# Kernel tuning notes

Measured on AMD Instinct MI355X. Metric: run time of the kernel, lower is better.

Reference implementation:

```python
import jax, jax.numpy as jnp
from jax import lax
import numpy as np

N_FEAT = 131072
N_TARGET = 2048
N_LATENT = 64
INNER_STEPS = 2
EPS = 1e-7


def setup_inputs() -> dict:
    key = jax.random.key(0)
    ks = jax.random.split(key, 10)
    x = jax.random.normal(ks[0], (N_FEAT,), jnp.float32)
    y = jax.random.normal(ks[1], (N_TARGET,), jnp.float32)
    mu_x = jax.random.normal(ks[2], (N_FEAT,), jnp.float32) * 0.01
    mu_y = jax.random.normal(ks[3], (N_TARGET,), jnp.float32) * 0.01
    u0 = jax.random.normal(ks[4], (N_LATENT,), jnp.float32)
    u = u0 / jnp.sqrt(jnp.sum(u0 * u0))
    Wz = jax.random.normal(ks[5], (N_LATENT, N_FEAT), jnp.float32) * 0.1
    Cz = jax.random.normal(ks[6], (N_LATENT, N_TARGET), jnp.float32) * 0.1
    t_sq_sum = jax.random.uniform(ks[7], (N_LATENT,), jnp.float32) * 10.0 + 1.0
    bz = jax.random.normal(ks[8], (N_LATENT,), jnp.float32) * 0.1
    P = jax.random.normal(ks[9], (N_LATENT, N_FEAT), jnp.float32) * 0.1
    return {"x": x, "y": y, "mu_x": mu_x, "mu_y": mu_y, "u": u, "Wz": Wz,
            "Cz": Cz, "t_sq_sum": t_sq_sum, "bz": bz, "P": P, "n": 100}


def _one_pass(u_i, wz_row, cz_row, tss, xc, yc):
    # one NIPALS inner iteration for latent i
    wz = wz_row + xc * u_i
    tz = jnp.dot(xc, wz) / (jnp.sqrt(jnp.sum(wz * wz)) + EPS)
    tss_ = tss + tz * tz
    t = tz / jnp.sqrt(tss_)
    cz = cz_row + yc * t
    C_i = cz / jnp.sqrt(jnp.sum(cz * cz))
    u_new = jnp.dot(yc, C_i)
    return u_new, wz, tz, tss_, t, cz, C_i


def reference(x, y, mu_x, mu_y, u, Wz, Cz, t_sq_sum, bz, P, n):
    # functional translation of IPLS.partial_fit (post burn-in branch, n > burn_in)
    nf = jnp.float32(n)
    mu_x_new = mu_x * (nf / (nf + 1.0)) + x / (nf + 1.0)
    mu_y_new = mu_y * (nf / (nf + 1.0)) + y / (nf + 1.0)
    xc = x - mu_x_new  # centered sample [n_feat]
    yc = y - mu_y_new  # centered target [n_target]

    def latent_step(carry, row):
        xc, yc = carry
        u_i, wz_row, cz_row, tss, bz_i, p_row = row
        u_i, wz, tz, tss_, t, cz, C_i = _one_pass(u_i, wz_row, cz_row, tss, xc, yc)
        for _ in range(INNER_STEPS - 1):
            u_i, wz, tz, tss_, t, cz, C_i = _one_pass(u_i, wz_row, cz_row, tss, xc, yc)
        bz_new = bz_i + u_i * tz
        b = bz_new / jnp.sqrt(tss_)
        p_new = p_row + xc * t
        xc = xc - t * p_new          # deflate x
        yc = yc - b * t * C_i        # deflate y
        return (xc, yc), (u_i, wz, cz, tss_, bz_new, p_new)

    (_, _), outs = lax.scan(latent_step, (xc, yc), (u, Wz, Cz, t_sq_sum, bz, P))
    u_new, Wz_new, Cz_new, tss_new, bz_new, P_new = outs
    return (mu_x_new, mu_y_new, u_new, Wz_new, Cz_new, tss_new, bz_new, P_new)
```

## Files before the change

kernel.cpp:

```cpp
#include <hip/hip_runtime.h>


#define NF 131072
#define NT 2048
#define NL 64

#define PSIZE 8385
#define NBX 512
#define NBY 16
#define NMID 32
#define REDK 16
#define BK 128
#define LDST 68
#define NBEX 256
#define NBEY 4

#define O_MUX 0
#define O_MUY 131072
#define O_U   133120
#define O_WZ  133184
#define O_CZ  8521792
#define O_TSS 8652864
#define O_BZ  8652928
#define O_P   8652992

#define W_FINX 0
#define W_FINY 8385
#define W_COEF 16770

__global__ __launch_bounds__(256) void gram_partial(
    const float* __restrict__ PX, const float* __restrict__ WzX,
    const float* __restrict__ xsX, const float* __restrict__ musX,
    const float* __restrict__ CzY, const float* __restrict__ ysY,
    const float* __restrict__ musY, const int* __restrict__ np,
    float* __restrict__ partX, float* __restrict__ voutX,
    float* __restrict__ partY, float* __restrict__ voutY)
{
    __shared__ float lds[2 * BK * LDST + BK];
    float* ldsA = lds;
    float* ldsB = lds + BK * LDST;
    float* ldsV = lds + 2 * BK * LDST;

    const bool isX = (int)blockIdx.x < NBX;
    const float* A   = isX ? PX   : CzY;
    const float* B   = isX ? WzX  : CzY;
    const float* xs  = isX ? xsX  : ysY;
    const float* mus = isX ? musX : musY;
    float* part      = isX ? partX : partY;
    float* vout      = isX ? voutX : voutY;
    const int K   = isX ? NF : NT;
    const int KC  = isX ? (NF / NBX) : (NT / NBY);
    const int bid = isX ? (int)blockIdx.x : (int)blockIdx.x - NBX;

    const int t    = threadIdx.x;
    const int w    = t >> 6;
    const int lane = t & 63;
    const int j0   = lane & 56;
    const int i0   = (lane & 7) << 3;

    const float nf = (float)(*np);
    const float r  = nf / (nf + 1.f);

    float accPW[8][8], accPP[8][8];
    float accXW[8], accXP[8], accW2[8], accS0 = 0.f;
#pragma unroll
    for (int s = 0; s < 8; ++s) {
        accXW[s] = 0.f; accXP[s] = 0.f; accW2[s] = 0.f;
#pragma unroll
        for (int q = 0; q < 8; ++q) { accPW[s][q] = 0.f; accPP[s][q] = 0.f; }
    }

    const int kbase  = bid * KC;
    const int ntiles = KC / BK;
    const int c4     = ((t >> 3) & 31) << 2;
    const int rlow   = t & 7;

    for (int tile = 0; tile < ntiles; ++tile) {
        const int k0 = kbase + tile * BK;
        if (tile) __syncthreads();
#pragma unroll
        for (int m = 0; m < 8; ++m) {
            int row = rlow | (m << 3);
            const float4 av = *(const float4*)(A + (size_t)row * K + (k0 + c4));
            const float4 bv = *(const float4*)(B + (size_t)row * K + (k0 + c4));
            ldsA[(c4 + 0) * LDST + row] = av.x;
            ldsA[(c4 + 1) * LDST + row] = av.y;
            ldsA[(c4 + 2) * LDST + row] = av.z;
            ldsA[(c4 + 3) * LDST + row] = av.w;
            ldsB[(c4 + 0) * LDST + row] = bv.x;
            ldsB[(c4 + 1) * LDST + row] = bv.y;
            ldsB[(c4 + 2) * LDST + row] = bv.z;
            ldsB[(c4 + 3) * LDST + row] = bv.w;
        }
        if (t < BK) {
            float val = r * (xs[k0 + t] - mus[k0 + t]);
            ldsV[t] = val;
            vout[k0 + t] = val;
        }
        __syncthreads();

        const int kend = w * 32 + 32;
        for (int kk = w * 32; kk < kend; ++kk) {
            const float* bA = ldsA + kk * LDST;
            const float* bB = ldsB + kk * LDST;
            float4 a0 = *(const float4*)(bA + j0);
            float4 a1 = *(const float4*)(bA + j0 + 4);
            float4 b0 = *(const float4*)(bB + i0);
            float4 b1 = *(const float4*)(bB + i0 + 4);
            float4 c0 = *(const float4*)(bA + i0);
            float4 c1 = *(const float4*)(bA + i0 + 4);
            float aj[8] = {a0.x,a0.y,a0.z,a0.w,a1.x,a1.y,a1.z,a1.w};
            float bi[8] = {b0.x,b0.y,b0.z,b0.w,b1.x,b1.y,b1.z,b1.w};
            float ci[8] = {c0.x,c0.y,c0.z,c0.w,c1.x,c1.y,c1.z,c1.w};
#pragma unroll
            for (int s = 0; s < 8; ++s)
#pragma unroll
                for (int q = 0; q < 8; ++q) {
                    accPW[s][q] = fmaf(aj[s], bi[q], accPW[s][q]);
                    accPP[s][q] = fmaf(aj[s], ci[q], accPP[s][q]);
                }
            float vv = ldsV[kk];
            if (j0 == 0) {
#pragma unroll
                for (int q = 0; q < 8; ++q) accXW[q] = fmaf(vv, bi[q], accXW[q]);
            }
            if (j0 == 8) {
#pragma unroll
                for (int q = 0; q < 8; ++q) accW2[q] = fmaf(bi[q], bi[q], accW2[q]);
            }
            if (i0 == 0) {
#pragma unroll
                for (int s = 0; s < 8; ++s) accXP[s] = fmaf(vv, aj[s], accXP[s]);
            }
            if (lane == 16) accS0 = fmaf(vv, vv, accS0);
        }
    }
    __syncthreads();

    float* red = lds;
    float* po  = part + (size_t)bid * PSIZE;
#pragma unroll
    for (int s = 0; s < 8; ++s)
#pragma unroll
        for (int q = 0; q < 8; ++q)
            red[w * 4096 + (j0 + s) * 64 + (i0 + q)] = accPW[s][q];
    __syncthreads();
    for (int o = t; o < 4096; o += 256)
        po[o] = red[o] + red[4096 + o] + red[8192 + o] + red[12288 + o];
    __syncthreads();
#pragma unroll
    for (int s = 0; s < 8; ++s)
#pragma unroll
        for (int q = 0; q < 8; ++q)
            red[w * 4096 + (j0 + s) * 64 + (i0 + q)] = accPP[s][q];
    __syncthreads();
    for (int o = t; o < 4096; o += 256)
        po[4096 + o] = red[o] + red[4096 + o] + red[8192 + o] + red[12288 + o];
    __syncthreads();
    if (j0 == 0) {
#pragma unroll
        for (int q = 0; q < 8; ++q) red[w * 193 + (i0 + q)] = accXW[q];
    }
    if (i0 == 0) {
#pragma unroll
        for (int s = 0; s < 8; ++s) red[w * 193 + 64 + (j0 + s)] = accXP[s];
    }
    if (j0 == 8) {
#pragma unroll
        for (int q = 0; q < 8; ++q) red[w * 193 + 128 + (i0 + q)] = accW2[q];
    }
    if (lane == 16) red[w * 193 + 192] = accS0;
    __syncthreads();
    for (int o = t; o < 193; o += 256)
        po[8192 + o] = red[o] + red[193 + o] + red[386 + o] + red[579 + o];
}

__global__ __launch_bounds__(256) void gram_reduceA(
    const float* __restrict__ partX, float* __restrict__ mid)
{
    int ob = (int)blockIdx.x % 33;
    int kb = (int)blockIdx.x / 33;
    int o  = ob * 256 + threadIdx.x;
    if (o >= PSIZE) return;
    const float* p = partX + (size_t)kb * REDK * PSIZE + o;
    float s = 0.f;
#pragma unroll
    for (int k = 0; k < REDK; ++k) s += p[(size_t)k * PSIZE];
    mid[(size_t)kb * PSIZE + o] = s;
}

__global__ __launch_bounds__(256) void gram_reduceB(
    const float* __restrict__ mid, const float* __restrict__ partY,
    float* __restrict__ finX, float* __restrict__ finY)
{
    int b = blockIdx.x;
    float s = 0.f;
    float* fin; int o;
    if (b < 33) {
        o = b * 256 + threadIdx.x;
        if (o >= PSIZE) return;
        fin = finX;
#pragma unroll
        for (int k = 0; k < NMID; ++k) s += mid[(size_t)k * PSIZE + o];
    } else {
        o = (b - 33) * 256 + threadIdx.x;
        if (o >= PSIZE) return;
        fin = finY;
#pragma unroll
        for (int k = 0; k < NBY; ++k) s += partY[(size_t)k * PSIZE + o];
    }
    if (o < 4096) {
        int j = o >> 6, i = o & 63;
        fin[(i << 6) + j] = s;
    } else if (o < 8192) {
        int q = o - 4096;
        int j = q >> 6, i = q & 63;
        fin[4096 + (i << 6) + j] = s;
    } else {
        fin[o] = s;
    }
}

__global__ __launch_bounds__(256) void recursion(
    const float* __restrict__ finX, const float* __restrict__ finY,
    const float* __restrict__ u_in, const float* __restrict__ tss_in,
    const float* __restrict__ bz_in,
    float* __restrict__ out_u, float* __restrict__ out_tss, float* __restrict__ out_bz,
    float* __restrict__ coef)
{
    __shared__ float lx[PSIZE];
    __shared__ float ly[PSIZE];
    __shared__ float lsc[3 * NL];

    const int t = threadIdx.x;
    for (int o = t; o < PSIZE; o += 256) { lx[o] = finX[o]; ly[o] = finY[o]; }
    if (t < NL) {
        lsc[t]          = u_in[t];
        lsc[NL + t]     = tss_in[t];
        lsc[2 * NL + t] = bz_in[t];
    }
    __syncthreads();
    if (t >= 64) return;
    const int lane = t;

    const float* PWt = lx;
    const float* PPt = lx + 4096;
    const float* XW  = lx + 8192;
    const float* XP  = lx + 8256;
    const float* W2  = lx + 8320;
    const float* CCt = ly;
    const float* YC  = ly + 8192;

    float beta = 0.f, delta = 0.f;
    float alpha = 1.f, gamma = 1.f;
    float s  = lx[8384];
    float sy = ly[8384];

    float rPW = PWt[lane], rPP = PPt[lane], rCC = CCt[lane];

    for (int i = 0; i < NL; ++i) {
        int inext = (i + 1) & 63;
        float nPW = PWt[inext * 64 + lane];
        float nPP = PPt[inext * 64 + lane];
        float nCC = CCt[inext * 64 + lane];

        float v0 = beta * rPW, v1 = beta * rPP, v2 = delta * rCC;
#pragma unroll
        for (int off = 32; off; off >>= 1) {
            v0 += __shfl_xor(v0, off);
            v1 += __shfl_xor(v1, off);
            v2 += __shfl_xor(v2, off);
        }
        float a  = alpha * XW[i] + v0;
        float d  = alpha * XP[i] + v1;
        float ay = gamma * YC[i] + v2;
        float ppii = __shfl(rPP, i);
        float c2   = __shfl(rCC, i);
        float w2   = W2[i];
        float u0 = lsc[i], tss0 = lsc[NL + i], bzi = lsc[2 * NL + i];

        float den1 = sqrtf(fmaxf(w2 + 2.f * u0 * a + u0 * u0 * s, 0.f)) + 1e-7f;
        float tz1  = (a + u0 * s) / den1;
        float tss1 = tss0 + tz1 * tz1;
        float t1   = tz1 / sqrtf(tss1);
        float cn1  = sqrtf(fmaxf(c2 + 2.f * t1 * ay + t1 * t1 * sy, 0.f));
        float u1   = (ay + t1 * sy) / cn1;
        float den2  = sqrtf(fmaxf(w2 + 2.f * u1 * a + u1 * u1 * s, 0.f)) + 1e-7f;
        float tz2   = (a + u1 * s) / den2;
        float tss2  = tss0 + tz2 * tz2;
        float st2   = sqrtf(tss2);
        float t2    = tz2 / st2;
        float cn2sq = fmaxf(c2 + 2.f * t2 * ay + t2 * t2 * sy, 0.f);
        float cn2   = sqrtf(cn2sq);
        float u2    = (ay + t2 * sy) / cn2;
        float bzo   = bzi + u2 * tz2;
        float b     = bzo / st2;
        float g     = b * t2 / cn2;

        if (lane == 0) {
            out_u[i]   = u2;
            out_tss[i] = tss2;
            out_bz[i]  = bzo;
            coef[i]            = u1;
            coef[NL + i]       = t2;
            coef[2 * NL + i]   = g;
        }

        float f  = 1.f - t2 * t2;
        float fy = 1.f - g * t2;
        s  = f * f * s - 2.f * f * t2 * d + t2 * t2 * ppii;
        sy = sy - 2.f * g * (ay + t2 * sy) + g * g * cn2sq;
        beta  *= f;  if (lane == i) beta  = -t2;
        delta *= fy; if (lane == i) delta = -g;
        alpha *= f;
        gamma *= fy;

        rPW = nPW; rPP = nPP; rCC = nCC;
    }
}

__global__ __launch_bounds__(128) void expand(
    const float* __restrict__ P, const float* __restrict__ Wz,
    const float* __restrict__ x, const float* __restrict__ Cz,
    const float* __restrict__ y, const float* __restrict__ coef,
    float* __restrict__ xc0_mux,
    float* __restrict__ yc0_muy,
    float* __restrict__ outW, float* __restrict__ outP, float* __restrict__ outC)
{
    __shared__ float cA[NL], cB[NL];
    const int t = threadIdx.x;
    const int b = (int)blockIdx.x;

    if (b < NBEX) {
        if (t < NL) { cA[t] = coef[t]; cB[t] = coef[NL + t]; }
        const int c = (b * 128 + t) << 2;
        float4 xc = *(const float4*)(xc0_mux + c);
        float4 xv = *(const float4*)(x + c);
        float4 mu;
        mu.x = xv.x - xc.x; mu.y = xv.y - xc.y;
        mu.z = xv.z - xc.z; mu.w = xv.w - xc.w;
        *(float4*)(xc0_mux + c) = mu;
        __syncthreads();
#pragma unroll 8
        for (int i = 0; i < NL; ++i) {
            size_t off = (size_t)i * NF + c;
            float4 wv = *(const float4*)(Wz + off);
            float4 pv = *(const float4*)(P + off);
            float u1 = cA[i], t2 = cB[i];
            wv.x = fmaf(u1, xc.x, wv.x); wv.y = fmaf(u1, xc.y, wv.y);
            wv.z = fmaf(u1, xc.z, wv.z); wv.w = fmaf(u1, xc.w, wv.w);
            pv.x = fmaf(t2, xc.x, pv.x); pv.y = fmaf(t2, xc.y, pv.y);
            pv.z = fmaf(t2, xc.z, pv.z); pv.w = fmaf(t2, xc.w, pv.w);
            *(float4*)(outW + off) = wv;
            *(float4*)(outP + off) = pv;
            xc.x = fmaf(-t2, pv.x, xc.x); xc.y = fmaf(-t2, pv.y, xc.y);
            xc.z = fmaf(-t2, pv.z, xc.z); xc.w = fmaf(-t2, pv.w, xc.w);
        }
    } else {
        if (t < NL) { cA[t] = coef[NL + t]; cB[t] = coef[2 * NL + t]; }
        const int c = ((b - NBEX) * 128 + t) << 2;
        float4 yc = *(const float4*)(yc0_muy + c);
        float4 yv = *(const float4*)(y + c);
        float4 mu;
        mu.x = yv.x - yc.x; mu.y = yv.y - yc.y;
        mu.z = yv.z - yc.z; mu.w = yv.w - yc.w;
        *(float4*)(yc0_muy + c) = mu;
        __syncthreads();
#pragma unroll 8
        for (int i = 0; i < NL; ++i) {
            size_t off = (size_t)i * NT + c;
            float4 cv = *(const float4*)(Cz + off);
            float t2 = cA[i], g = cB[i];
            cv.x = fmaf(t2, yc.x, cv.x); cv.y = fmaf(t2, yc.y, cv.y);
            cv.z = fmaf(t2, yc.z, cv.z); cv.w = fmaf(t2, yc.w, cv.w);
            *(float4*)(outC + off) = cv;
            yc.x = fmaf(-g, cv.x, yc.x); yc.y = fmaf(-g, cv.y, yc.y);
            yc.z = fmaf(-g, cv.z, yc.z); yc.w = fmaf(-g, cv.w, yc.w);
        }
    }
}

extern "C" void kernel_launch(void* const* d_in, const int* in_sizes, int n_in,
                              void* d_out, int out_size, void* d_ws, size_t ws_size,
                              hipStream_t stream)
{
    (void)in_sizes; (void)n_in; (void)out_size; (void)ws_size;

    const float* x    = (const float*)d_in[0];
    const float* y    = (const float*)d_in[1];
    const float* mu_x = (const float*)d_in[2];
    const float* mu_y = (const float*)d_in[3];
    const float* u    = (const float*)d_in[4];
    const float* Wz   = (const float*)d_in[5];
    const float* Cz   = (const float*)d_in[6];
    const float* tss  = (const float*)d_in[7];
    const float* bz   = (const float*)d_in[8];
    const float* P    = (const float*)d_in[9];
    const int*   n    = (const int*)d_in[10];

    float* out = (float*)d_out;
    float* ws  = (float*)d_ws;

    float* xc0   = out + O_MUX;
    float* yc0   = out + O_MUY;
    float* partX = out + O_P;
    float* partY = partX + (size_t)NBX * PSIZE;
    float* mid   = partY + (size_t)NBY * PSIZE;
    float* finX  = ws + W_FINX;
    float* finY  = ws + W_FINY;
    float* coef  = ws + W_COEF;

    gram_partial<<<NBX + NBY, 256, 0, stream>>>(P, Wz, x, mu_x,
                                                Cz, y, mu_y, n,
                                                partX, xc0, partY, yc0);

    gram_reduceA<<<33 * NMID, 256, 0, stream>>>(partX, mid);
    gram_reduceB<<<66, 256, 0, stream>>>(mid, partY, finX, finY);

    recursion<<<1, 256, 0, stream>>>(finX, finY, u, tss, bz,
                                     out + O_U, out + O_TSS, out + O_BZ, coef);

    expand<<<NBEX + NBEY, 128, 0, stream>>>(P, Wz, x, Cz, y, coef,
                                            xc0, yc0,
                                            out + O_WZ, out + O_P, out + O_CZ);
}
```

Measured before the change: 261.1 us.

## Double gram partial blocks, rework recursion with readlane, and scalarize expand

The X gram pass now runs on 1024 blocks with a 64-wide k tile and occupancy hints, and the Y gram moves to a separate launch. The partial buffers are split across two output regions, and reduceB drops its transpose by writing results in natural order. The recursion replaces shuffle reductions with incrementally updated per-lane vectors, uses readlane broadcasts and fast rcp/rsq approximations, and writes outputs once at the end. The expand kernel switches from float4 to scalar accesses with 256 threads per block. Together these aim for more parallelism and a shorter serial recursion, at the cost of more partial traffic and slight precision loss from the approximate reciprocals.

```diff
diff --git a/kernel.cpp b/kernel.cpp
--- a/kernel.cpp
+++ b/kernel.cpp
@@ -6,14 +6,12 @@
 #define NL 64
 
 #define PSIZE 8385
-#define NBX 512
+#define NBX 1024
 #define NBY 16
-#define NMID 32
+#define NMID 64
 #define REDK 16
-#define BK 128
+#define BK 64
 #define LDST 68
-#define NBEX 256
-#define NBEY 4
 
 #define O_MUX 0
 #define O_MUY 131072
@@ -28,29 +26,23 @@
 #define W_FINY 8385
 #define W_COEF 16770
 
-__global__ __launch_bounds__(256) void gram_partial(
-    const float* __restrict__ PX, const float* __restrict__ WzX,
-    const float* __restrict__ xsX, const float* __restrict__ musX,
-    const float* __restrict__ CzY, const float* __restrict__ ysY,
-    const float* __restrict__ musY, const int* __restrict__ np,
-    float* __restrict__ partX, float* __restrict__ voutX,
-    float* __restrict__ partY, float* __restrict__ voutY)
+__device__ __forceinline__ float rdlane(float v, int l) {
+    return __int_as_float(__builtin_amdgcn_readlane(__float_as_int(v), l));
+}
+#define FRCP(x) __builtin_amdgcn_rcpf(x)
+#define FRSQ(x) __builtin_amdgcn_rsqf(x)
+
+__global__ __launch_bounds__(256, 4) void gram_partial(
+    const float* __restrict__ A, const float* __restrict__ B,
+    const float* __restrict__ xs, const float* __restrict__ mus,
+    const int* __restrict__ np, int K, int KC,
+    float* __restrict__ part0, float* __restrict__ part1,
+    float* __restrict__ vout)
 {
     __shared__ float lds[2 * BK * LDST + BK];
     float* ldsA = lds;
     float* ldsB = lds + BK * LDST;
     float* ldsV = lds + 2 * BK * LDST;
-
-    const bool isX = (int)blockIdx.x < NBX;
-    const float* A   = isX ? PX   : CzY;
-    const float* B   = isX ? WzX  : CzY;
-    const float* xs  = isX ? xsX  : ysY;
-    const float* mus = isX ? musX : musY;
-    float* part      = isX ? partX : partY;
-    float* vout      = isX ? voutX : voutY;
-    const int K   = isX ? NF : NT;
-    const int KC  = isX ? (NF / NBX) : (NT / NBY);
-    const int bid = isX ? (int)blockIdx.x : (int)blockIdx.x - NBX;
 
     const int t    = threadIdx.x;
     const int w    = t >> 6;
@@ -70,17 +62,18 @@
         for (int q = 0; q < 8; ++q) { accPW[s][q] = 0.f; accPP[s][q] = 0.f; }
     }
 
+    const int bid    = (int)blockIdx.x;
     const int kbase  = bid * KC;
     const int ntiles = KC / BK;
-    const int c4     = ((t >> 3) & 31) << 2;
-    const int rlow   = t & 7;
+    const int rbase = (t & 7) | ((t >> 4) & 8);
+    const int c4    = ((t >> 3) & 15) << 2;
 
     for (int tile = 0; tile < ntiles; ++tile) {
         const int k0 = kbase + tile * BK;
         if (tile) __syncthreads();
 #pragma unroll
-        for (int m = 0; m < 8; ++m) {
-            int row = rlow | (m << 3);
+        for (int m = 0; m < 4; ++m) {
+            int row = rbase | (m << 4);
             const float4 av = *(const float4*)(A + (size_t)row * K + (k0 + c4));
             const float4 bv = *(const float4*)(B + (size_t)row * K + (k0 + c4));
             ldsA[(c4 + 0) * LDST + row] = av.x;
@@ -99,8 +92,8 @@
         }
         __syncthreads();
 
-        const int kend = w * 32 + 32;
-        for (int kk = w * 32; kk < kend; ++kk) {
+        const int kend = w * 16 + 16;
+        for (int kk = w * 16; kk < kend; ++kk) {
             const float* bA = ldsA + kk * LDST;
             const float* bB = ldsB + kk * LDST;
             float4 a0 = *(const float4*)(bA + j0);
@@ -138,24 +131,51 @@
     __syncthreads();
 
     float* red = lds;
-    float* po  = part + (size_t)bid * PSIZE;
-#pragma unroll
-    for (int s = 0; s < 8; ++s)
-#pragma unroll
-        for (int q = 0; q < 8; ++q)
-            red[w * 4096 + (j0 + s) * 64 + (i0 + q)] = accPW[s][q];
-    __syncthreads();
-    for (int o = t; o < 4096; o += 256)
-        po[o] = red[o] + red[4096 + o] + red[8192 + o] + red[12288 + o];
-    __syncthreads();
-#pragma unroll
-    for (int s = 0; s < 8; ++s)
-#pragma unroll
-        for (int q = 0; q < 8; ++q)
-            red[w * 4096 + (j0 + s) * 64 + (i0 + q)] = accPP[s][q];
-    __syncthreads();
-    for (int o = t; o < 4096; o += 256)
-        po[4096 + o] = red[o] + red[4096 + o] + red[8192 + o] + red[12288 + o];
+    float* po  = (bid < 512 ? part0 : part1) + (size_t)(bid & 511) * PSIZE;
+
+    if (j0 < 32) {
+#pragma unroll
+        for (int s = 0; s < 8; ++s)
+#pragma unroll
+            for (int q = 0; q < 8; ++q)
+                red[w * 2048 + (j0 + s) * 64 + (i0 + q)] = accPW[s][q];
+    }
+    __syncthreads();
+    for (int o = t; o < 2048; o += 256)
+        po[o] = red[o] + red[2048 + o] + red[4096 + o] + red[6144 + o];
+    __syncthreads();
+    if (j0 >= 32) {
+#pragma unroll
+        for (int s = 0; s < 8; ++s)
+#pragma unroll
+            for (int q = 0; q < 8; ++q)
+                red[w * 2048 + (j0 - 32 + s) * 64 + (i0 + q)] = accPW[s][q];
+    }
+    __syncthreads();
+    for (int o = t; o < 2048; o += 256)
+        po[2048 + o] = red[o] + red[2048 + o] + red[4096 + o] + red[6144 + o];
+    __syncthreads();
+    if (j0 < 32) {
+#pragma unroll
+        for (int s = 0; s < 8; ++s)
+#pragma unroll
+            for (int q = 0; q < 8; ++q)
+                red[w * 2048 + (j0 + s) * 64 + (i0 + q)] = accPP[s][q];
+    }
+    __syncthreads();
+    for (int o = t; o < 2048; o += 256)
+        po[4096 + o] = red[o] + red[2048 + o] + red[4096 + o] + red[6144 + o];
+    __syncthreads();
+    if (j0 >= 32) {
+#pragma unroll
+        for (int s = 0; s < 8; ++s)
+#pragma unroll
+            for (int q = 0; q < 8; ++q)
+                red[w * 2048 + (j0 - 32 + s) * 64 + (i0 + q)] = accPP[s][q];
+    }
+    __syncthreads();
+    for (int o = t; o < 2048; o += 256)
+        po[6144 + o] = red[o] + red[2048 + o] + red[4096 + o] + red[6144 + o];
     __syncthreads();
     if (j0 == 0) {
 #pragma unroll
@@ -176,13 +196,15 @@
 }
 
 __global__ __launch_bounds__(256) void gram_reduceA(
-    const float* __restrict__ partX, float* __restrict__ mid)
+    const float* __restrict__ part0, const float* __restrict__ part1,
+    float* __restrict__ mid)
 {
     int ob = (int)blockIdx.x % 33;
     int kb = (int)blockIdx.x / 33;
     int o  = ob * 256 + threadIdx.x;
     if (o >= PSIZE) return;
-    const float* p = partX + (size_t)kb * REDK * PSIZE + o;
+    const float* p = (kb < 32 ? part0 : part1)
+                   + (size_t)((kb & 31) * REDK) * PSIZE + o;
     float s = 0.f;
 #pragma unroll
     for (int k = 0; k < REDK; ++k) s += p[(size_t)k * PSIZE];
@@ -194,30 +216,20 @@
     float* __restrict__ finX, float* __restrict__ finY)
 {
     int b = blockIdx.x;
-    float s = 0.f;
-    float* fin; int o;
     if (b < 33) {
-        o = b * 256 + threadIdx.x;
+        int o = b * 256 + threadIdx.x;
         if (o >= PSIZE) return;
-        fin = finX;
+        float s = 0.f;
 #pragma unroll
         for (int k = 0; k < NMID; ++k) s += mid[(size_t)k * PSIZE + o];
+        finX[o] = s;
     } else {
-        o = (b - 33) * 256 + threadIdx.x;
+        int o = (b - 33) * 256 + threadIdx.x;
         if (o >= PSIZE) return;
-        fin = finY;
+        float s = 0.f;
 #pragma unroll
         for (int k = 0; k < NBY; ++k) s += partY[(size_t)k * PSIZE + o];
-    }
-    if (o < 4096) {
-        int j = o >> 6, i = o & 63;
-        fin[(i << 6) + j] = s;
-    } else if (o < 8192) {
-        int q = o - 4096;
-        int j = q >> 6, i = q & 63;
-        fin[4096 + (i << 6) + j] = s;
-    } else {
-        fin[o] = s;
+        finY[o] = s;
     }
 }
 
@@ -243,83 +255,81 @@
     if (t >= 64) return;
     const int lane = t;
 
-    const float* PWt = lx;
-    const float* PPt = lx + 4096;
-    const float* XW  = lx + 8192;
-    const float* XP  = lx + 8256;
-    const float* W2  = lx + 8320;
-    const float* CCt = ly;
-    const float* YC  = ly + 8192;
-
-    float beta = 0.f, delta = 0.f;
-    float alpha = 1.f, gamma = 1.f;
+    const float* PW = lx;
+    const float* PP = lx + 4096;
+    const float* CC = ly;
+
+    float A   = lx[8192 + lane];
+    float D   = lx[8256 + lane];
+    float AY  = ly[8192 + lane];
+    float w2r = lx[8320 + lane];
+    float u0r = lsc[lane], tssr = lsc[NL + lane], bzr = lsc[2 * NL + lane];
     float s  = lx[8384];
     float sy = ly[8384];
 
-    float rPW = PWt[lane], rPP = PPt[lane], rCC = CCt[lane];
+    float rPW = PW[lane], rPP = PP[lane], rCC = CC[lane];
+    float o_u = 0.f, o_tss = 0.f, o_bz = 0.f, o_u1 = 0.f, o_t2 = 0.f, o_g = 0.f;
 
     for (int i = 0; i < NL; ++i) {
         int inext = (i + 1) & 63;
-        float nPW = PWt[inext * 64 + lane];
-        float nPP = PPt[inext * 64 + lane];
-        float nCC = CCt[inext * 64 + lane];
-
-        float v0 = beta * rPW, v1 = beta * rPP, v2 = delta * rCC;
-#pragma unroll
-        for (int off = 32; off; off >>= 1) {
-            v0 += __shfl_xor(v0, off);
-            v1 += __shfl_xor(v1, off);
-            v2 += __shfl_xor(v2, off);
-        }
-        float a  = alpha * XW[i] + v0;
-        float d  = alpha * XP[i] + v1;
-        float ay = gamma * YC[i] + v2;
-        float ppii = __shfl(rPP, i);
-        float c2   = __shfl(rCC, i);
-        float w2   = W2[i];
-        float u0 = lsc[i], tss0 = lsc[NL + i], bzi = lsc[2 * NL + i];
+        float nPW = PW[inext * 64 + lane];
+        float nPP = PP[inext * 64 + lane];
+        float nCC = CC[inext * 64 + lane];
+
+        float a    = rdlane(A, i);
+        float d    = rdlane(D, i);
+        float ay   = rdlane(AY, i);
+        float ppii = rdlane(rPP, i);
+        float c2   = rdlane(rCC, i);
+        float w2   = rdlane(w2r, i);
+        float u0   = rdlane(u0r, i);
+        float tss0 = rdlane(tssr, i);
+        float bzi  = rdlane(bzr, i);
 
         float den1 = sqrtf(fmaxf(w2 + 2.f * u0 * a + u0 * u0 * s, 0.f)) + 1e-7f;
-        float tz1  = (a + u0 * s) / den1;
+        float tz1  = (a + u0 * s) * FRCP(den1);
         float tss1 = tss0 + tz1 * tz1;
-        float t1   = tz1 / sqrtf(tss1);
+        float t1   = tz1 * FRSQ(tss1);
         float cn1  = sqrtf(fmaxf(c2 + 2.f * t1 * ay + t1 * t1 * sy, 0.f));
-        float u1   = (ay + t1 * sy) / cn1;
+        float u1   = (ay + t1 * sy) * FRCP(cn1);
         float den2  = sqrtf(fmaxf(w2 + 2.f * u1 * a + u1 * u1 * s, 0.f)) + 1e-7f;
-        float tz2   = (a + u1 * s) / den2;
+        float tz2   = (a + u1 * s) * FRCP(den2);
         float tss2  = tss0 + tz2 * tz2;
-        float st2   = sqrtf(tss2);
-        float t2    = tz2 / st2;
+        float rs2   = FRSQ(tss2);
+        float t2    = tz2 * rs2;
         float cn2sq = fmaxf(c2 + 2.f * t2 * ay + t2 * t2 * sy, 0.f);
         float cn2   = sqrtf(cn2sq);
-        float u2    = (ay + t2 * sy) / cn2;
+        float rcn2  = FRCP(cn2);
+        float u2    = (ay + t2 * sy) * rcn2;
         float bzo   = bzi + u2 * tz2;
-        float b     = bzo / st2;
-        float g     = b * t2 / cn2;
-
-        if (lane == 0) {
-            out_u[i]   = u2;
-            out_tss[i] = tss2;
-            out_bz[i]  = bzo;
-            coef[i]            = u1;
-            coef[NL + i]       = t2;
-            coef[2 * NL + i]   = g;
+        float b     = bzo * rs2;
+        float g     = b * t2 * rcn2;
+
+        if (lane == i) {
+            o_u = u2; o_tss = tss2; o_bz = bzo;
+            o_u1 = u1; o_t2 = t2; o_g = g;
         }
 
         float f  = 1.f - t2 * t2;
         float fy = 1.f - g * t2;
         s  = f * f * s - 2.f * f * t2 * d + t2 * t2 * ppii;
         sy = sy - 2.f * g * (ay + t2 * sy) + g * g * cn2sq;
-        beta  *= f;  if (lane == i) beta  = -t2;
-        delta *= fy; if (lane == i) delta = -g;
-        alpha *= f;
-        gamma *= fy;
+        A  = fmaf(-t2, rPW, f * A);
+        D  = fmaf(-t2, rPP, f * D);
+        AY = fmaf(-g,  rCC, fy * AY);
 
         rPW = nPW; rPP = nPP; rCC = nCC;
     }
-}
-
-__global__ __launch_bounds__(128) void expand(
+
+    out_u[lane]   = o_u;
+    out_tss[lane] = o_tss;
+    out_bz[lane]  = o_bz;
+    coef[lane]          = o_u1;
+    coef[NL + lane]     = o_t2;
+    coef[2 * NL + lane] = o_g;
+}
+
+__global__ __launch_bounds__(256) void expand(
     const float* __restrict__ P, const float* __restrict__ Wz,
     const float* __restrict__ x, const float* __restrict__ Cz,
     const float* __restrict__ y, const float* __restrict__ coef,
@@ -331,51 +341,35 @@
     const int t = threadIdx.x;
     const int b = (int)blockIdx.x;
 
-    if (b < NBEX) {
+    if (b < 512) {
         if (t < NL) { cA[t] = coef[t]; cB[t] = coef[NL + t]; }
-        const int c = (b * 128 + t) << 2;
-        float4 xc = *(const float4*)(xc0_mux + c);
-        float4 xv = *(const float4*)(x + c);
-        float4 mu;
-        mu.x = xv.x - xc.x; mu.y = xv.y - xc.y;
-        mu.z = xv.z - xc.z; mu.w = xv.w - xc.w;
-        *(float4*)(xc0_mux + c) = mu;
+        const int c = b * 256 + t;
+        float xc = xc0_mux[c];
+        xc0_mux[c] = x[c] - xc;
         __syncthreads();
 #pragma unroll 8
         for (int i = 0; i < NL; ++i) {
             size_t off = (size_t)i * NF + c;
-            float4 wv = *(const float4*)(Wz + off);
-            float4 pv = *(const float4*)(P + off);
-            float u1 = cA[i], t2 = cB[i];
-            wv.x = fmaf(u1, xc.x, wv.x); wv.y = fmaf(u1, xc.y, wv.y);
-            wv.z = fmaf(u1, xc.z, wv.z); wv.w = fmaf(u1, xc.w, wv.w);
-            pv.x = fmaf(t2, xc.x, pv.x); pv.y = fmaf(t2, xc.y, pv.y);
-            pv.z = fmaf(t2, xc.z, pv.z); pv.w = fmaf(t2, xc.w, pv.w);
-            *(float4*)(outW + off) = wv;
-            *(float4*)(outP + off) = pv;
-            xc.x = fmaf(-t2, pv.x, xc.x); xc.y = fmaf(-t2, pv.y, xc.y);
-            xc.z = fmaf(-t2, pv.z, xc.z); xc.w = fmaf(-t2, pv.w, xc.w);
+            float wv = Wz[off], pv = P[off];
+            wv = fmaf(cA[i], xc, wv);
+            pv = fmaf(cB[i], xc, pv);
+            outW[off] = wv;
+            outP[off] = pv;
+            xc = fmaf(-cB[i], pv, xc);
         }
     } else {
         if (t < NL) { cA[t] = coef[NL + t]; cB[t] = coef[2 * NL + t]; }
-        const int c = ((b - NBEX) * 128 + t) << 2;
-        float4 yc = *(const float4*)(yc0_muy + c);
-        float4 yv = *(const float4*)(y + c);
-        float4 mu;
-        mu.x = yv.x - yc.x; mu.y = yv.y - yc.y;
-        mu.z = yv.z - yc.z; mu.w = yv.w - yc.w;
-        *(float4*)(yc0_muy + c) = mu;
+        const int c = (b - 512) * 256 + t;
+        float yc = yc0_muy[c];
+        yc0_muy[c] = y[c] - yc;
         __syncthreads();
 #pragma unroll 8
         for (int i = 0; i < NL; ++i) {
             size_t off = (size_t)i * NT + c;
-            float4 cv = *(const float4*)(Cz + off);
-            float t2 = cA[i], g = cB[i];
-            cv.x = fmaf(t2, yc.x, cv.x); cv.y = fmaf(t2, yc.y, cv.y);
-            cv.z = fmaf(t2, yc.z, cv.z); cv.w = fmaf(t2, yc.w, cv.w);
-            *(float4*)(outC + off) = cv;
-            yc.x = fmaf(-g, cv.x, yc.x); yc.y = fmaf(-g, cv.y, yc.y);
-            yc.z = fmaf(-g, cv.z, yc.z); yc.w = fmaf(-g, cv.w, yc.w);
+            float cv = Cz[off];
+            cv = fmaf(cA[i], yc, cv);
+            outC[off] = cv;
+            yc = fmaf(-cB[i], cv, yc);
         }
     }
 }
@@ -403,24 +397,26 @@
 
     float* xc0   = out + O_MUX;
     float* yc0   = out + O_MUY;
-    float* partX = out + O_P;
-    float* partY = partX + (size_t)NBX * PSIZE;
-    float* mid   = partY + (size_t)NBY * PSIZE;
+    float* part0 = out + O_P;
+    float* mid   = part0 + (size_t)512 * PSIZE;
+    float* partY = mid   + (size_t)NMID * PSIZE;
+    float* part1 = out + O_WZ;
     float* finX  = ws + W_FINX;
     float* finY  = ws + W_FINY;
     float* coef  = ws + W_COEF;
 
-    gram_partial<<<NBX + NBY, 256, 0, stream>>>(P, Wz, x, mu_x,
-                                                Cz, y, mu_y, n,
-                                                partX, xc0, partY, yc0);
-
-    gram_reduceA<<<33 * NMID, 256, 0, stream>>>(partX, mid);
+    gram_partial<<<NBX, 256, 0, stream>>>(P,  Wz, x, mu_x, n, NF, NF / NBX,
+                                          part0, part1, xc0);
+    gram_partial<<<NBY, 256, 0, stream>>>(Cz, Cz, y, mu_y, n, NT, NT / NBY,
+                                          partY, partY, yc0);
+
+    gram_reduceA<<<33 * NMID, 256, 0, stream>>>(part0, part1, mid);
     gram_reduceB<<<66, 256, 0, stream>>>(mid, partY, finX, finY);
 
     recursion<<<1, 256, 0, stream>>>(finX, finY, u, tss, bz,
                                      out + O_U, out + O_TSS, out + O_BZ, coef);
 
-    expand<<<NBEX + NBEY, 128, 0, stream>>>(P, Wz, x, Cz, y, coef,
-                                            xc0, yc0,
-                                            out + O_WZ, out + O_P, out + O_CZ);
-}
+    expand<<<520, 256, 0, stream>>>(P, Wz, x, Cz, y, coef,
+                                    xc0, yc0,
+                                    out + O_WZ, out + O_P, out + O_CZ);
+}
```

Measured after the change: 930.3 us. 256% more time.
